# Optimization experiments

Hardware: AMD Instinct MI355X
Metric: run time of the kernel (lower is better)

## Reference

```python
import jax, jax.numpy as jnp
import numpy as np
from jax.scipy.special import xlogy

N = 12288
DATA_LEN = 50000
MARGIN = 1.0
GAMMA = 0.1
LAMBDA = 1.0
EPS = 1e-12


def setup_inputs() -> dict:
    key = jax.random.key(0)
    k1, k2, k3 = jax.random.split(key, 3)
    y_pred = jax.random.uniform(k1, (N, 1), dtype=jnp.float32)
    y_pred_adv = jax.random.uniform(k2, (N, 1), dtype=jnp.float32)
    y_true = jax.random.randint(k3, (N,), 0, 2)
    index_s = jnp.arange(N)
    u_all = jnp.zeros((DATA_LEN, 1), dtype=jnp.float32)
    u_pos = jnp.zeros((DATA_LEN, 1), dtype=jnp.float32)
    return {"y_pred": y_pred, "y_pred_adv": y_pred_adv, "u_all": u_all,
            "u_pos": u_pos, "y_true": y_true, "index_s": index_s}


def reference(y_pred, y_pred_adv, u_all, u_pos, y_true, index_s):
    sg = jax.lax.stop_gradient
    f = y_pred[:, 0]                       # [N]
    pos = (y_true == 1)                    # [N] bool
    posf = pos.astype(f.dtype)             # [N]
    # pairwise squared hinge: rows = positives (masked later), cols = all samples
    sur = jnp.square(jnp.maximum(MARGIN - (f[:, None] - f[None, :]), 0.0))  # [N,N]
    row_mean = jnp.mean(sur, axis=1)                       # mean over all samples
    pos_row_mean = jnp.mean(sur * posf[None, :], axis=1)   # mean over positives-as-zeros
    # moving-average buffer update (detached), only at positive rows' indices
    ua = u_all[index_s, 0]
    up = u_pos[index_s, 0]
    ua_new = jnp.where(pos, (1.0 - GAMMA) * ua + GAMMA * sg(row_mean), ua)
    up_new = jnp.where(pos, (1.0 - GAMMA) * up + GAMMA * sg(pos_row_mean), up)
    # p_ij = (u_pos_i - u_all_i * pos_mask_j) / u_all_i^2, detached, rows masked to positives
    denom = jnp.where(pos, jnp.square(ua_new), 1.0)        # guard 0 division on neg rows
    p = (up_new[:, None] - ua_new[:, None] * posf[None, :]) / denom[:, None]
    p = sg(p) * posf[:, None]
    n_pos = jnp.sum(posf)
    nat_loss = jnp.sum(p * sur) / (n_pos * f.shape[0])     # mean over P x N elements
    # adversarial KL (batchmean over first dim)
    y_prob = jnp.concatenate([y_pred, 1.0 - y_pred], axis=-1)          # [N,2]
    y_prob_adv = jnp.concatenate([y_pred_adv, 1.0 - y_pred_adv], axis=-1)
    log_in = jnp.log(y_prob_adv + EPS)
    adv_loss = jnp.sum(xlogy(y_prob, y_prob) - y_prob * log_in) / y_prob.shape[0]
    return nat_loss + LAMBDA * adv_loss
```

## Files before the change

### kernel.cpp

```cpp
#include <hip/hip_runtime.h>
#include <math.h>

#define LAMBDA 1.0
#define EPS 1e-12f

constexpr int BLK  = 512;
constexpr int MAXB = 64;
constexpr unsigned FLAG_SET = 0x13371337u;


__global__ __launch_bounds__(BLK)
void adap_one_kernel(const float* __restrict__ y_pred,
                     const float* __restrict__ y_pred_adv,
                     const float* __restrict__ u_all,
                     const float* __restrict__ u_pos,
                     const int*  __restrict__ y_true,
                     const int*  __restrict__ index_s,
                     double* __restrict__ part,
                     unsigned* __restrict__ flag1,
                     unsigned* __restrict__ flag2,
                     float* __restrict__ out,
                     int n) {
    __shared__ double swred[BLK / 64][8];
    __shared__ double sh[8];

    const int nb   = gridDim.x;
    const int b    = blockIdx.x;
    const int lane = threadIdx.x & 63;
    const int wave = threadIdx.x >> 6;
    const int i    = b * BLK + threadIdx.x;

    double v0 = 0, v1 = 0, v2 = 0, v3 = 0, v4 = 0, v5 = 0;
    float  f = 0.0f;
    int    pos = 0;
    double ua = 0.0, up = 0.0;
    if (i < n) {
        f   = y_pred[i];
        pos = (y_true[i] == 1);
        const double fd = (double)f;
        v0 = fd; v1 = fd * fd;
        if (pos) {
            v2 = fd; v3 = fd * fd; v4 = 1.0;
            const int idx = index_s[i];
            ua = (double)u_all[idx];
            up = (double)u_pos[idx];
        }
        const float p  = f;
        const float q  = 1.0f - f;
        const float pa = y_pred_adv[i];
        const float qa = 1.0f - pa;
        float t = 0.0f;
        if (p > 0.0f) t += p * logf(p);
        if (q > 0.0f) t += q * logf(q);
        t -= p * logf(pa + EPS);
        t -= q * logf(qa + EPS);
        v5 = (double)t;
    }

    for (int off = 32; off > 0; off >>= 1) {
        v0 += __shfl_down(v0, off, 64);
        v1 += __shfl_down(v1, off, 64);
        v2 += __shfl_down(v2, off, 64);
        v3 += __shfl_down(v3, off, 64);
        v4 += __shfl_down(v4, off, 64);
        v5 += __shfl_down(v5, off, 64);
    }
    if (lane == 0) {
        swred[wave][0] = v0; swred[wave][1] = v1; swred[wave][2] = v2;
        swred[wave][3] = v3; swred[wave][4] = v4; swred[wave][5] = v5;
    }
    __syncthreads();
    if (threadIdx.x < 6) {
        double a = 0.0;
        #pragma unroll
        for (int w = 0; w < BLK / 64; ++w) a += swred[w][threadIdx.x];
        sh[threadIdx.x] = a;
    }
    __syncthreads();

    if (threadIdx.x == 0) {
        #pragma unroll
        for (int s = 0; s < 6; ++s)
            __hip_atomic_store(&part[b * 8 + s], sh[s],
                               __ATOMIC_RELAXED, __HIP_MEMORY_SCOPE_AGENT);
        __hip_atomic_store(&flag1[b], FLAG_SET,
                           __ATOMIC_RELEASE, __HIP_MEMORY_SCOPE_AGENT);
    }

    if (wave == 0 && lane < nb) {
        while (__hip_atomic_load(&flag1[lane], __ATOMIC_ACQUIRE,
                                 __HIP_MEMORY_SCOPE_AGENT) != FLAG_SET)
            __builtin_amdgcn_s_sleep(1);
    }
    __syncthreads();

    if (wave < 6) {
        double x = (lane < nb)
            ? __hip_atomic_load(&part[lane * 8 + wave], __ATOMIC_RELAXED,
                                __HIP_MEMORY_SCOPE_AGENT)
            : 0.0;
        for (int off = 32; off > 0; off >>= 1) x += __shfl_down(x, off, 64);
        if (lane == 0) sh[wave] = x;
    }
    __syncthreads();
    const double S1 = sh[0], S2 = sh[1], S1p = sh[2], S2p = sh[3];
    const double Np = sh[4], adv = sh[5];

    double csum = 0.0;
    const double nd = (double)n;
    if (i < n && pos) {
        const double a = 1.0 - (double)f;
        const double row_sum     = nd * a * a + 2.0 * a * S1  + S2;
        const double pos_row_sum = Np * a * a + 2.0 * a * S1p + S2p;
        const double ua_new = 0.9 * ua + 0.1 * (row_sum / nd);
        const double up_new = 0.9 * up + 0.1 * (pos_row_sum / nd);
        csum = (up_new * row_sum - ua_new * pos_row_sum) / (ua_new * ua_new);
    }
    for (int off = 32; off > 0; off >>= 1) csum += __shfl_down(csum, off, 64);
    if (lane == 0) swred[wave][0] = csum;
    __syncthreads();
    if (threadIdx.x == 0) {
        double a = 0.0;
        #pragma unroll
        for (int w = 0; w < BLK / 64; ++w) a += swred[w][0];
        __hip_atomic_store(&part[b * 8 + 6], a,
                           __ATOMIC_RELAXED, __HIP_MEMORY_SCOPE_AGENT);
        __hip_atomic_store(&flag2[b], FLAG_SET,
                           __ATOMIC_RELEASE, __HIP_MEMORY_SCOPE_AGENT);
    }

    if (b == 0) {
        if (wave == 0 && lane < nb) {
            while (__hip_atomic_load(&flag2[lane], __ATOMIC_ACQUIRE,
                                     __HIP_MEMORY_SCOPE_AGENT) != FLAG_SET)
                __builtin_amdgcn_s_sleep(1);
        }
        __syncthreads();
        if (wave == 0) {
            double x = (lane < nb)
                ? __hip_atomic_load(&part[lane * 8 + 6], __ATOMIC_RELAXED,
                                    __HIP_MEMORY_SCOPE_AGENT)
                : 0.0;
            for (int off = 32; off > 0; off >>= 1) x += __shfl_down(x, off, 64);
            if (lane == 0) {
                const double nat_loss = x / (Np * nd);
                const double adv_loss = adv / nd;
                out[0] = (float)(nat_loss + LAMBDA * adv_loss);
            }
        }
    }
}

extern "C" void kernel_launch(void* const* d_in, const int* in_sizes, int n_in,
                              void* d_out, int out_size, void* d_ws, size_t ws_size,
                              hipStream_t stream) {
    const float* y_pred     = (const float*)d_in[0];
    const float* y_pred_adv = (const float*)d_in[1];
    const float* u_all      = (const float*)d_in[2];
    const float* u_pos      = (const float*)d_in[3];
    const int*   y_true     = (const int*)d_in[4];
    const int*   index_s    = (const int*)d_in[5];
    float* out = (float*)d_out;
    const int n = in_sizes[0];

    double*   part  = (double*)d_ws;
    unsigned* flag1 = (unsigned*)((char*)d_ws + MAXB * 8 * sizeof(double));
    unsigned* flag2 = flag1 + MAXB;

    const int nb = (n + BLK - 1) / BLK;

    adap_one_kernel<<<nb, BLK, 0, stream>>>(y_pred, y_pred_adv, u_all, u_pos,
                                            y_true, index_s, part, flag1, flag2,
                                            out, n);
}
```

Before: 68.63 us.

## Collapse multi-block flag-synchronized reduction into a single 1024-thread block

Replaces the multi-block kernel, which synchronized through global-memory flags and spin-waits, with a single 1024-thread block. Each thread now strides over up to 12 elements in both passes, so the moment sums and the final loss are reduced entirely in shared memory. This removes the inter-block spin barriers, the global partial stores and the workspace use. In exchange, only one compute unit does the loads and log evaluations, and the second pass re-reads y_true, y_pred and the u buffers.

```diff
diff --git a/kernel.cpp b/kernel.cpp
--- a/kernel.cpp
+++ b/kernel.cpp
@@ -4,47 +4,33 @@
 #define LAMBDA 1.0
 #define EPS 1e-12f
 
-constexpr int BLK  = 512;
-constexpr int MAXB = 64;
-constexpr unsigned FLAG_SET = 0x13371337u;
-
+constexpr int BLK      = 1024;
+constexpr int MAX_ITER = 12;
 
 __global__ __launch_bounds__(BLK)
-void adap_one_kernel(const float* __restrict__ y_pred,
-                     const float* __restrict__ y_pred_adv,
-                     const float* __restrict__ u_all,
-                     const float* __restrict__ u_pos,
-                     const int*  __restrict__ y_true,
-                     const int*  __restrict__ index_s,
-                     double* __restrict__ part,
-                     unsigned* __restrict__ flag1,
-                     unsigned* __restrict__ flag2,
-                     float* __restrict__ out,
-                     int n) {
+void adap_one_block(const float* __restrict__ y_pred,
+                    const float* __restrict__ y_pred_adv,
+                    const float* __restrict__ u_all,
+                    const float* __restrict__ u_pos,
+                    const int*  __restrict__ y_true,
+                    const int*  __restrict__ index_s,
+                    float* __restrict__ out,
+                    int n) {
     __shared__ double swred[BLK / 64][8];
     __shared__ double sh[8];
 
-    const int nb   = gridDim.x;
-    const int b    = blockIdx.x;
-    const int lane = threadIdx.x & 63;
-    const int wave = threadIdx.x >> 6;
-    const int i    = b * BLK + threadIdx.x;
+    const int tid  = threadIdx.x;
+    const int lane = tid & 63;
+    const int wave = tid >> 6;
 
     double v0 = 0, v1 = 0, v2 = 0, v3 = 0, v4 = 0, v5 = 0;
-    float  f = 0.0f;
-    int    pos = 0;
-    double ua = 0.0, up = 0.0;
-    if (i < n) {
-        f   = y_pred[i];
-        pos = (y_true[i] == 1);
+
+    auto body1 = [&](int i) {
+        const float f   = y_pred[i];
+        const int   pos = (y_true[i] == 1);
         const double fd = (double)f;
-        v0 = fd; v1 = fd * fd;
-        if (pos) {
-            v2 = fd; v3 = fd * fd; v4 = 1.0;
-            const int idx = index_s[i];
-            ua = (double)u_all[idx];
-            up = (double)u_pos[idx];
-        }
+        v0 += fd; v1 += fd * fd;
+        if (pos) { v2 += fd; v3 += fd * fd; v4 += 1.0; }
         const float p  = f;
         const float q  = 1.0f - f;
         const float pa = y_pred_adv[i];
@@ -54,8 +40,15 @@
         if (q > 0.0f) t += q * logf(q);
         t -= p * logf(pa + EPS);
         t -= q * logf(qa + EPS);
-        v5 = (double)t;
+        v5 += (double)t;
+    };
+
+    #pragma unroll
+    for (int k = 0; k < MAX_ITER; ++k) {
+        const int i = k * BLK + tid;
+        if (i < n) body1(i);
     }
+    for (int i = MAX_ITER * BLK + tid; i < n; i += BLK) body1(i);
 
     for (int off = 32; off > 0; off >>= 1) {
         v0 += __shfl_down(v0, off, 64);
@@ -70,37 +63,11 @@
         swred[wave][3] = v3; swred[wave][4] = v4; swred[wave][5] = v5;
     }
     __syncthreads();
-    if (threadIdx.x < 6) {
+    if (tid < 6) {
         double a = 0.0;
         #pragma unroll
-        for (int w = 0; w < BLK / 64; ++w) a += swred[w][threadIdx.x];
-        sh[threadIdx.x] = a;
-    }
-    __syncthreads();
-
-    if (threadIdx.x == 0) {
-        #pragma unroll
-        for (int s = 0; s < 6; ++s)
-            __hip_atomic_store(&part[b * 8 + s], sh[s],
-                               __ATOMIC_RELAXED, __HIP_MEMORY_SCOPE_AGENT);
-        __hip_atomic_store(&flag1[b], FLAG_SET,
-                           __ATOMIC_RELEASE, __HIP_MEMORY_SCOPE_AGENT);
-    }
-
-    if (wave == 0 && lane < nb) {
-        while (__hip_atomic_load(&flag1[lane], __ATOMIC_ACQUIRE,
-                                 __HIP_MEMORY_SCOPE_AGENT) != FLAG_SET)
-            __builtin_amdgcn_s_sleep(1);
-    }
-    __syncthreads();
-
-    if (wave < 6) {
-        double x = (lane < nb)
-            ? __hip_atomic_load(&part[lane * 8 + wave], __ATOMIC_RELAXED,
-                                __HIP_MEMORY_SCOPE_AGENT)
-            : 0.0;
-        for (int off = 32; off > 0; off >>= 1) x += __shfl_down(x, off, 64);
-        if (lane == 0) sh[wave] = x;
+        for (int w = 0; w < BLK / 64; ++w) a += swred[w][tid];
+        sh[tid] = a;
     }
     __syncthreads();
     const double S1 = sh[0], S2 = sh[1], S1p = sh[2], S2p = sh[3];
@@ -108,46 +75,40 @@
 
     double csum = 0.0;
     const double nd = (double)n;
-    if (i < n && pos) {
-        const double a = 1.0 - (double)f;
-        const double row_sum     = nd * a * a + 2.0 * a * S1  + S2;
-        const double pos_row_sum = Np * a * a + 2.0 * a * S1p + S2p;
-        const double ua_new = 0.9 * ua + 0.1 * (row_sum / nd);
-        const double up_new = 0.9 * up + 0.1 * (pos_row_sum / nd);
-        csum = (up_new * row_sum - ua_new * pos_row_sum) / (ua_new * ua_new);
+
+    auto body2 = [&](int i) {
+        if (y_true[i] == 1) {
+            const double f = (double)y_pred[i];
+            const int  idx = index_s[i];
+            const double ua = (double)u_all[idx];
+            const double up = (double)u_pos[idx];
+            const double a  = 1.0 - f;
+            const double row_sum     = nd * a * a + 2.0 * a * S1  + S2;
+            const double pos_row_sum = Np * a * a + 2.0 * a * S1p + S2p;
+            const double ua_new = 0.9 * ua + 0.1 * (row_sum / nd);
+            const double up_new = 0.9 * up + 0.1 * (pos_row_sum / nd);
+            csum += (up_new * row_sum - ua_new * pos_row_sum) / (ua_new * ua_new);
+        }
+    };
+
+    #pragma unroll
+    for (int k = 0; k < MAX_ITER; ++k) {
+        const int i = k * BLK + tid;
+        if (i < n) body2(i);
     }
+    for (int i = MAX_ITER * BLK + tid; i < n; i += BLK) body2(i);
+
     for (int off = 32; off > 0; off >>= 1) csum += __shfl_down(csum, off, 64);
     if (lane == 0) swred[wave][0] = csum;
     __syncthreads();
-    if (threadIdx.x == 0) {
+
+    if (tid == 0) {
         double a = 0.0;
         #pragma unroll
         for (int w = 0; w < BLK / 64; ++w) a += swred[w][0];
-        __hip_atomic_store(&part[b * 8 + 6], a,
-                           __ATOMIC_RELAXED, __HIP_MEMORY_SCOPE_AGENT);
-        __hip_atomic_store(&flag2[b], FLAG_SET,
-                           __ATOMIC_RELEASE, __HIP_MEMORY_SCOPE_AGENT);
-    }
-
-    if (b == 0) {
-        if (wave == 0 && lane < nb) {
-            while (__hip_atomic_load(&flag2[lane], __ATOMIC_ACQUIRE,
-                                     __HIP_MEMORY_SCOPE_AGENT) != FLAG_SET)
-                __builtin_amdgcn_s_sleep(1);
-        }
-        __syncthreads();
-        if (wave == 0) {
-            double x = (lane < nb)
-                ? __hip_atomic_load(&part[lane * 8 + 6], __ATOMIC_RELAXED,
-                                    __HIP_MEMORY_SCOPE_AGENT)
-                : 0.0;
-            for (int off = 32; off > 0; off >>= 1) x += __shfl_down(x, off, 64);
-            if (lane == 0) {
-                const double nat_loss = x / (Np * nd);
-                const double adv_loss = adv / nd;
-                out[0] = (float)(nat_loss + LAMBDA * adv_loss);
-            }
-        }
+        const double nat_loss = a / (Np * nd);
+        const double adv_loss = adv / nd;
+        out[0] = (float)(nat_loss + LAMBDA * adv_loss);
     }
 }
 
@@ -163,13 +124,8 @@
     float* out = (float*)d_out;
     const int n = in_sizes[0];
 
-    double*   part  = (double*)d_ws;
-    unsigned* flag1 = (unsigned*)((char*)d_ws + MAXB * 8 * sizeof(double));
-    unsigned* flag2 = flag1 + MAXB;
+    (void)d_ws; (void)ws_size;
 
-    const int nb = (n + BLK - 1) / BLK;
-
-    adap_one_kernel<<<nb, BLK, 0, stream>>>(y_pred, y_pred_adv, u_all, u_pos,
-                                            y_true, index_s, part, flag1, flag2,
-                                            out, n);
+    adap_one_block<<<1, BLK, 0, stream>>>(y_pred, y_pred_adv, u_all, u_pos,
+                                          y_true, index_s, out, n);
 }
```

New measurement: 81.85 us. 1.19x slower.
